# Optimization experiments

Measured on AMD Instinct MI355X. Metric: run time of the kernel, lower is better.

Reference implementation:

```python
import jax, jax.numpy as jnp
import numpy as np

B, D, E, H, K = 8192, 1024, 8, 4096, 2

def setup_inputs() -> dict:
    key = jax.random.key(0)
    ks = jax.random.split(key, 7)
    s_in = 1.0 / np.sqrt(D)
    s_hid = 1.0 / np.sqrt(H)
    return {
        "z":  jax.random.normal(ks[0], (B, D), dtype=jnp.float32),
        "Wg": jax.random.uniform(ks[1], (D, E), jnp.float32, -s_in, s_in),
        "bg": jnp.zeros((E,), jnp.float32),
        "W1": jax.random.uniform(ks[2], (E, D, H), jnp.float32, -s_in, s_in),
        "b1": jax.random.uniform(ks[3], (E, H), jnp.float32, -s_in, s_in),
        "W2": jax.random.uniform(ks[4], (E, H, D), jnp.float32, -s_hid, s_hid),
        "b2": jax.random.uniform(ks[5], (E, D), jnp.float32, -s_hid, s_hid),
    }

def reference(z, Wg, bg, W1, b1, W2, b2):
    # gate: softmax over experts, then keep only top-k weights (no renorm,
    # matching the original which sums topw * expert(z))
    w = jax.nn.softmax(z @ Wg + bg, axis=-1)            # [B, E]
    topw, idx = jax.lax.top_k(w, K)                      # [B, K] each
    wmask = jnp.zeros_like(w).at[jnp.arange(B)[:, None], idx].set(topw)  # [B, E]
    # dense all-expert MLP, then weighted combine (same math as per-token loop)
    h = jax.nn.relu(jnp.einsum('bd,edh->beh', z, W1) + b1)   # [B, E, H]
    y = jnp.einsum('beh,ehd->bed', h, W2) + b2               # [B, E, D]
    out = jnp.einsum('be,bed->bd', wmask, y)                 # [B, D]
    return out
```

## Files before the change

kernel.cpp:

```cpp
#include <hip/hip_runtime.h>
#include <hip/hip_bf16.h>
#include <cstdint>
#include <cstddef>

#define BTOK  8192
#define DIM   1024
#define NEXP  8
#define NHID  4096
#define HHALF 2048
#define GATE_TOK 64
#define ABASE (128 * 32)

typedef __bf16 bf16x8 __attribute__((ext_vector_type(8)));
typedef float  floatx4 __attribute__((ext_vector_type(4)));

#define O_COUNTS 0
#define O_BASE   256
#define O_TOKB   1024
#define O_TOKW   (O_TOKB + (size_t)NEXP*BTOK*4)
#define O_CE     (O_TOKW + (size_t)NEXP*BTOK*4)
#define O_CP     (O_CE + (size_t)2*BTOK*4)
#define O_CW     (O_CP + (size_t)2*BTOK*4)
#define O_ZBF    (O_CW + (size_t)2*BTOK*4)
#define O_W1T    (O_ZBF + (size_t)BTOK*DIM*2)
#define O_W2T    (O_W1T + (size_t)NEXP*DIM*NHID*2)
#define O_HBUF   (O_W2T + (size_t)NEXP*DIM*NHID*2)
#define WS_NEED  (O_HBUF + (size_t)2*BTOK*NHID*2)

__device__ __forceinline__ void gload_lds16(const void* g, void* l) {
  __builtin_amdgcn_global_load_lds(
      (const __attribute__((address_space(1))) void*)g,
      (__attribute__((address_space(3))) void*)l, 16, 0, 0);
}

__device__ __forceinline__ ushort f2bf(float x) {
  return __builtin_bit_cast(ushort, __float2bfloat16(x));
}

__global__ void k_zcnt(int* __restrict__ counts) {
  if (threadIdx.x < 12) counts[threadIdx.x] = 0;
}

__global__ void k_zout(float* __restrict__ out) {
  int i = blockIdx.x * blockDim.x + threadIdx.x;
  float4 z4 = {0.f, 0.f, 0.f, 0.f};
  float4* o = (float4*)out;
  int n = BTOK * DIM / 4;
  for (int j = i; j < n; j += gridDim.x * blockDim.x) o[j] = z4;
}

__global__ __launch_bounds__(256) void k_transpose(
    const float* __restrict__ src, __hip_bfloat16* __restrict__ dst, int R, int C) {
  __shared__ float tile[32][33];
  int zz = blockIdx.z;
  const float* s = src + (size_t)zz * R * C;
  __hip_bfloat16* d = dst + (size_t)zz * R * C;
  int c0 = blockIdx.x * 32, r0 = blockIdx.y * 32;
  int tx = threadIdx.x & 31, ty = threadIdx.x >> 5;
#pragma unroll
  for (int i = ty; i < 32; i += 8)
    tile[i][tx] = s[(size_t)(r0 + i) * C + c0 + tx];
  __syncthreads();
#pragma unroll
  for (int i = ty; i < 32; i += 8)
    d[(size_t)(c0 + i) * R + r0 + tx] = __float2bfloat16(tile[tx][i]);
}

__global__ __launch_bounds__(256) void k_gate(
    const float* __restrict__ z, const float* __restrict__ Wg,
    const float* __restrict__ bg, int* __restrict__ counts,
    int* __restrict__ tokb, float* __restrict__ tokw,
    __hip_bfloat16* __restrict__ zbf) {
  __shared__ float wgT[NEXP * DIM];
  __shared__ int   le[2 * GATE_TOK];
  __shared__ float lw[2 * GATE_TOK];
  __shared__ int   lr[2 * GATE_TOK];
  __shared__ int   lcnt[NEXP];
  __shared__ int   gbase[NEXP];

  int tid = threadIdx.x;
  if (tid < NEXP) lcnt[tid] = 0;
#pragma unroll
  for (int e = 0; e < NEXP; e++)
    for (int d = tid; d < DIM; d += 256)
      wgT[e * DIM + d] = Wg[d * NEXP + e];
  __syncthreads();

  int lane = tid & 63;
  int wv = tid >> 6;
  int b0 = blockIdx.x * GATE_TOK;

  for (int t = 0; t < 16; t++) {
    int lt = wv * 16 + t;
    int b = b0 + lt;
    const float4* zr4 = (const float4*)(z + (size_t)b * DIM);
    float4 zv[4];
#pragma unroll
    for (int i = 0; i < 4; i++) zv[i] = zr4[lane + 64 * i];
    ushort4* zb4 = (ushort4*)((ushort*)zbf + (size_t)b * DIM);
#pragma unroll
    for (int i = 0; i < 4; i++) {
      ushort4 u;
      u.x = f2bf(zv[i].x); u.y = f2bf(zv[i].y);
      u.z = f2bf(zv[i].z); u.w = f2bf(zv[i].w);
      zb4[lane + 64 * i] = u;
    }
    float acc[NEXP];
#pragma unroll
    for (int e = 0; e < NEXP; e++) acc[e] = 0.f;
#pragma unroll
    for (int e = 0; e < NEXP; e++) {
      const float4* wg4 = (const float4*)(wgT + e * DIM);
#pragma unroll
      for (int i = 0; i < 4; i++) {
        float4 w4 = wg4[lane + 64 * i];
        acc[e] += zv[i].x * w4.x + zv[i].y * w4.y + zv[i].z * w4.z + zv[i].w * w4.w;
      }
    }
#pragma unroll
    for (int off = 32; off > 0; off >>= 1) {
#pragma unroll
      for (int e = 0; e < NEXP; e++) acc[e] += __shfl_down(acc[e], off);
    }
    if (lane == 0) {
      float mx = -1e30f;
#pragma unroll
      for (int e = 0; e < NEXP; e++) { acc[e] += bg[e]; mx = fmaxf(mx, acc[e]); }
      float s = 0.f;
#pragma unroll
      for (int e = 0; e < NEXP; e++) { acc[e] = expf(acc[e] - mx); s += acc[e]; }
      float inv = 1.f / s;
      int i1 = -1, i2 = -1; float v1 = -1.f, v2 = -1.f;
#pragma unroll
      for (int e = 0; e < NEXP; e++) {
        float w = acc[e] * inv;
        if (w > v1) { v2 = v1; i2 = i1; v1 = w; i1 = e; }
        else if (w > v2) { v2 = w; i2 = e; }
      }
      le[2 * lt] = i1;     lw[2 * lt] = v1;
      le[2 * lt + 1] = i2; lw[2 * lt + 1] = v2;
    }
  }
  __syncthreads();
  if (tid < 2 * GATE_TOK) lr[tid] = atomicAdd(&lcnt[le[tid]], 1);
  __syncthreads();
  if (tid < NEXP) gbase[tid] = atomicAdd(&counts[tid], lcnt[tid]);
  __syncthreads();
  if (tid < 2 * GATE_TOK) {
    int e = le[tid];
    int p = gbase[e] + lr[tid];
    int b = b0 + (tid >> 1);
    tokb[e * BTOK + p] = b;
    tokw[e * BTOK + p] = lw[tid];
  }
}

__global__ void k_base(const int* __restrict__ counts, int* __restrict__ base) {
  if (threadIdx.x == 0 && blockIdx.x == 0) {
    int s = 0;
    for (int e = 0; e < NEXP; e++) { base[e] = s; s += counts[e]; }
    int a = 0, b = 0;
    base[8] = 0; base[17] = 0;
    for (int e = 0; e < NEXP; e++) {
      int mt = (counts[e] + 127) >> 7;
      a += mt * 16; b += mt * 4;
      base[9 + e] = a; base[18 + e] = b;
    }
  }
}


#define STG3(nxt_, tt_) do {                                                 \
    gload_lds16(srcA  + (tt_) * 32, &lds[nxt_][(wv * 16) * 32]);             \
    gload_lds16(srcB0 + (tt_) * 32, &lds[nxt_][ABASE + (wv * 16) * 32]);     \
    gload_lds16(srcB1 + (tt_) * 32, &lds[nxt_][ABASE + (128 + wv * 16) * 32]);\
  } while (0)

#define PH3(cur_, STG_, VM_) do {                                            \
    const ushort* Ab_ = &lds[cur_][0];                                       \
    const ushort* Bb_ = &lds[cur_][ABASE];                                   \
    bf16x8 afr_[4], bfr_[4];                                                 \
    _Pragma("unroll")                                                        \
    for (int j_ = 0; j_ < 4; j_++)                                           \
      bfr_[j_] = __builtin_bit_cast(bf16x8,                                  \
          *(const uint4*)(Bb_ + boff + j_ * 512));                           \
    _Pragma("unroll")                                                        \
    for (int i_ = 0; i_ < 4; i_++)                                           \
      afr_[i_] = __builtin_bit_cast(bf16x8,                                  \
          *(const uint4*)(Ab_ + aoff + i_ * 512));                           \
    STG_;                                                                    \
    __builtin_amdgcn_sched_barrier(0);                                       \
    VM_;                                                                     \
    __builtin_amdgcn_s_barrier();                                            \
    __builtin_amdgcn_sched_barrier(0);                                       \
    __builtin_amdgcn_s_setprio(1);                                           \
    _Pragma("unroll")                                                        \
    for (int i_ = 0; i_ < 4; i_++)                                           \
      _Pragma("unroll")                                                      \
      for (int j_ = 0; j_ < 4; j_++)                                         \
        acc[i_][j_] = __builtin_amdgcn_mfma_f32_16x16x32_bf16(               \
            afr_[i_], bfr_[j_], acc[i_][j_], 0, 0, 0);                       \
    __builtin_amdgcn_s_setprio(0);                                           \
    __builtin_amdgcn_sched_barrier(0);                                       \
    __builtin_amdgcn_s_barrier();                                            \
  } while (0)

#define VM3  asm volatile("s_waitcnt vmcnt(3)" ::: "memory")
#define VM0  asm volatile("s_waitcnt vmcnt(0)" ::: "memory")
#define NOP_ (void)0

__global__ __launch_bounds__(512, 4) void k_gemm1(
    const __hip_bfloat16* __restrict__ zbf, const __hip_bfloat16* __restrict__ w1t,
    const float* __restrict__ b1, const int* __restrict__ counts,
    const int* __restrict__ base, const int* __restrict__ tokb,
    __hip_bfloat16* __restrict__ hbuf,
    const int* __restrict__ tp, int* __restrict__ steal) {
  __shared__ __align__(16) ushort lds[3][(128 + 256) * 32];
  __shared__ int sh_g;

  int tid = threadIdx.x;
  int lane = tid & 63;
  int wv = tid >> 6;
  int wm = wv >> 2;
  int wn = wv & 3;
  int lrow = lane & 15;
  int quad = lane >> 4;
  int pc = quad ^ ((lrow >> 1) & 3);
  int aoff = (wm * 64 + lrow) * 32 + pc * 8;
  int boff = (wn * 64 + lrow) * 32 + pc * 8;
  int srow = wv * 16 + (lane >> 2);
  int sswz = ((lane & 3) ^ ((srow >> 1) & 3)) * 8;

  const ushort* zb = (const ushort*)zbf;
  const ushort* w1 = (const ushort*)w1t;
  const int NT = DIM / 32;
  int TT = tp[8];

  for (;;) {
    if (tid == 0) sh_g = atomicAdd(steal, 1);
    __syncthreads();
    int g = sh_g;
    if (g >= TT) break;

    int e = 0;
    while (g >= tp[e + 1]) e++;
    int local = g - tp[e];
    int mte = (tp[e + 1] - tp[e]) >> 4;
    int nt = local / mte;
    int mtl = local - nt * mte;
    int m0 = mtl * 128, n0 = nt * 256;
    int cnt = counts[e], gb = base[e];

    int m = m0 + srow; if (m >= cnt) m = cnt - 1;
    const ushort* srcA = zb + (size_t)tokb[e * BTOK + m] * DIM + sswz;
    const ushort* srcB0 = w1 + (size_t)(e * NHID + n0 + srow) * DIM + sswz;
    const ushort* srcB1 = w1 + (size_t)(e * NHID + n0 + 128 + srow) * DIM + sswz;

    STG3(0, 0);
    STG3(1, 1);
    VM3;
    __builtin_amdgcn_s_barrier();

    floatx4 acc[4][4];
#pragma unroll
    for (int i = 0; i < 4; i++)
#pragma unroll
      for (int j = 0; j < 4; j++) { floatx4 zf = {0.f,0.f,0.f,0.f}; acc[i][j] = zf; }

    int cur = 0;
#pragma unroll 1
    for (int t = 0; t < NT - 2; ++t) {
      int nxt = cur + 2; if (nxt >= 3) nxt -= 3;
      PH3(cur, STG3(nxt, t + 2), VM3);
      cur = (cur == 2) ? 0 : cur + 1;
    }
    PH3(cur, NOP_, VM0);
    cur = (cur == 2) ? 0 : cur + 1;
    PH3(cur, NOP_, NOP_);

    float bias[4];
#pragma unroll
    for (int j = 0; j < 4; j++)
      bias[j] = b1[e * NHID + n0 + wn * 64 + j * 16 + lrow];
    ushort* hp = (ushort*)hbuf;
#pragma unroll
    for (int i = 0; i < 4; i++) {
      int mloc = wm * 64 + i * 16 + quad * 4;
#pragma unroll
      for (int r = 0; r < 4; r++) {
        int mm = m0 + mloc + r;
        if (mm < cnt) {
          ushort* hr = hp + (size_t)(gb + mm) * NHID;
#pragma unroll
          for (int j = 0; j < 4; j++) {
            float v = fmaxf(acc[i][j][r] + bias[j], 0.f);
            hr[n0 + wn * 64 + j * 16 + lrow] = f2bf(v);
          }
        }
      }
    }
    __syncthreads();
  }
}

__global__ __launch_bounds__(512, 4) void k_gemm2(
    const __hip_bfloat16* __restrict__ hbuf, const __hip_bfloat16* __restrict__ w2t,
    const float* __restrict__ b2, const int* __restrict__ counts,
    const int* __restrict__ base, const int* __restrict__ tokb,
    const float* __restrict__ tokw, float* __restrict__ out,
    const int* __restrict__ tp, int* __restrict__ steal) {
  __shared__ __align__(16) ushort lds[3][(128 + 256) * 32];
  __shared__ int sh_g;

  int tid = threadIdx.x;
  int lane = tid & 63;
  int wv = tid >> 6;
  int wm = wv >> 2;
  int wn = wv & 3;
  int lrow = lane & 15;
  int quad = lane >> 4;
  int pc = quad ^ ((lrow >> 1) & 3);
  int aoff = (wm * 64 + lrow) * 32 + pc * 8;
  int boff = (wn * 64 + lrow) * 32 + pc * 8;
  int srow = wv * 16 + (lane >> 2);
  int sswz = ((lane & 3) ^ ((srow >> 1) & 3)) * 8;

  const ushort* hb = (const ushort*)hbuf;
  const ushort* w2 = (const ushort*)w2t;
  const int NT = HHALF / 32;
  int TT = tp[8];

  for (;;) {
    if (tid == 0) sh_g = atomicAdd(steal, 1);
    __syncthreads();
    int gu = sh_g;
    if (gu >= 2 * TT) break;
    int g = gu >> 1;
    int kseg = gu & 1;

    int e = 0;
    while (g >= tp[e + 1]) e++;
    int local = g - tp[e];
    int mte = (tp[e + 1] - tp[e]) >> 2;
    int nt = local / mte;
    int mtl = local - nt * mte;
    int m0 = mtl * 128, n0 = nt * 256;
    int cnt = counts[e], gb = base[e];

    int m = m0 + srow; if (m >= cnt) m = cnt - 1;
    const ushort* srcA = hb + (size_t)(gb + m) * NHID + kseg * HHALF + sswz;
    const ushort* srcB0 = w2 + (size_t)(e * DIM + n0 + srow) * NHID + kseg * HHALF + sswz;
    const ushort* srcB1 = w2 + (size_t)(e * DIM + n0 + 128 + srow) * NHID + kseg * HHALF + sswz;

    STG3(0, 0);
    STG3(1, 1);
    VM3;
    __builtin_amdgcn_s_barrier();

    floatx4 acc[4][4];
#pragma unroll
    for (int i = 0; i < 4; i++)
#pragma unroll
      for (int j = 0; j < 4; j++) { floatx4 zf = {0.f,0.f,0.f,0.f}; acc[i][j] = zf; }

    int cur = 0;
#pragma unroll 1
    for (int t = 0; t < NT - 2; ++t) {
      int nxt = cur + 2; if (nxt >= 3) nxt -= 3;
      PH3(cur, STG3(nxt, t + 2), VM3);
      cur = (cur == 2) ? 0 : cur + 1;
    }
    PH3(cur, NOP_, VM0);
    cur = (cur == 2) ? 0 : cur + 1;
    PH3(cur, NOP_, NOP_);

#pragma unroll
    for (int i = 0; i < 4; i++) {
      int mloc = wm * 64 + i * 16 + quad * 4;
#pragma unroll
      for (int r = 0; r < 4; r++) {
        int mm = m0 + mloc + r;
        if (mm < cnt) {
          int tk  = tokb[e * BTOK + mm];
          float w = tokw[e * BTOK + mm];
#pragma unroll
          for (int j = 0; j < 4; j++) {
            int n = n0 + wn * 64 + j * 16 + lrow;
            float v = acc[i][j][r] + (kseg == 0 ? b2[e * DIM + n] : 0.f);
            atomicAdd(&out[(size_t)tk * DIM + n], w * v);
          }
        }
      }
    }
    __syncthreads();
  }
}

extern "C" void kernel_launch(void* const* d_in, const int* in_sizes, int n_in,
                              void* d_out, int out_size, void* d_ws, size_t ws_size,
                              hipStream_t stream) {
  const float* z  = (const float*)d_in[0];
  const float* Wg = (const float*)d_in[1];
  const float* bg = (const float*)d_in[2];
  const float* W1 = (const float*)d_in[3];
  const float* b1 = (const float*)d_in[4];
  const float* W2 = (const float*)d_in[5];
  const float* b2 = (const float*)d_in[6];
  float* out = (float*)d_out;
  char* ws = (char*)d_ws;
  if (ws_size < WS_NEED) return;

  int*   counts = (int*)(ws + O_COUNTS);
  int*   base   = (int*)(ws + O_BASE);
  int*   tokb   = (int*)(ws + O_TOKB);
  float* tokw   = (float*)(ws + O_TOKW);
  __hip_bfloat16* zbf  = (__hip_bfloat16*)(ws + O_ZBF);
  __hip_bfloat16* w1t  = (__hip_bfloat16*)(ws + O_W1T);
  __hip_bfloat16* w2t  = (__hip_bfloat16*)(ws + O_W2T);
  __hip_bfloat16* hbuf = (__hip_bfloat16*)(ws + O_HBUF);

  k_zcnt<<<1, 64, 0, stream>>>(counts);
  k_zout<<<512, 256, 0, stream>>>(out);
  k_transpose<<<dim3(NHID / 32, DIM / 32, NEXP), 256, 0, stream>>>(W1, w1t, DIM, NHID);
  k_transpose<<<dim3(DIM / 32, NHID / 32, NEXP), 256, 0, stream>>>(W2, w2t, NHID, DIM);
  k_gate<<<BTOK / GATE_TOK, 256, 0, stream>>>(z, Wg, bg, counts, tokb, tokw, zbf);
  k_base<<<1, 64, 0, stream>>>(counts, base);
  k_gemm1<<<512, 512, 0, stream>>>(
      zbf, w1t, b1, counts, base, tokb, hbuf, base + 8, counts + 8);
  k_gemm2<<<512, 512, 0, stream>>>(
      hbuf, w2t, b2, counts, base, tokb, tokw, out, base + 17, counts + 9);
}
```

Measured before the change: 879.3 us.

## Shrink GEMM tiles to 128x128 with 4-wave blocks and restructure LDS pipeline

Both expert GEMMs change from 512-thread blocks computing 128x256 tiles to 256-thread blocks computing 128x128 tiles. There are twice as many tiles, the persistent grid grows to 768 blocks, and the per-expert tile prefix counts in k_base are updated to match. Each stage now issues four 16-byte global-to-LDS loads per thread, and the wait and barrier move ahead of the fragment reads with adjusted vmcnt thresholds. The aim is finer load balance and more independent blocks per CU. The cost is lower reuse of each loaded A/B tile, so more global traffic per FLOP.

```diff
diff --git a/kernel.cpp b/kernel.cpp
--- a/kernel.cpp
+++ b/kernel.cpp
@@ -163,20 +163,26 @@
     base[8] = 0; base[17] = 0;
     for (int e = 0; e < NEXP; e++) {
       int mt = (counts[e] + 127) >> 7;
-      a += mt * 16; b += mt * 4;
+      a += mt * 32; b += mt * 8;
       base[9 + e] = a; base[18 + e] = b;
     }
   }
 }
 
 
-#define STG3(nxt_, tt_) do {                                                 \
-    gload_lds16(srcA  + (tt_) * 32, &lds[nxt_][(wv * 16) * 32]);             \
-    gload_lds16(srcB0 + (tt_) * 32, &lds[nxt_][ABASE + (wv * 16) * 32]);     \
-    gload_lds16(srcB1 + (tt_) * 32, &lds[nxt_][ABASE + (128 + wv * 16) * 32]);\
+#define STG4(nxt_, tt_) do {                                                  \
+    gload_lds16(srcA0 + (tt_) * 32, &lds[nxt_][(wv * 16) * 32]);              \
+    gload_lds16(srcA1 + (tt_) * 32, &lds[nxt_][(64 + wv * 16) * 32]);         \
+    gload_lds16(srcB0 + (tt_) * 32, &lds[nxt_][ABASE + (wv * 16) * 32]);      \
+    gload_lds16(srcB1 + (tt_) * 32, &lds[nxt_][ABASE + (64 + wv * 16) * 32]); \
   } while (0)
 
-#define PH3(cur_, STG_, VM_) do {                                            \
+#define PHR(cur_, STG_, VM_) do {                                            \
+    STG_;                                                                    \
+    __builtin_amdgcn_sched_barrier(0);                                       \
+    VM_;                                                                     \
+    __builtin_amdgcn_s_barrier();                                            \
+    __builtin_amdgcn_sched_barrier(0);                                       \
     const ushort* Ab_ = &lds[cur_][0];                                       \
     const ushort* Bb_ = &lds[cur_][ABASE];                                   \
     bf16x8 afr_[4], bfr_[4];                                                 \
@@ -188,11 +194,6 @@
     for (int i_ = 0; i_ < 4; i_++)                                           \
       afr_[i_] = __builtin_bit_cast(bf16x8,                                  \
           *(const uint4*)(Ab_ + aoff + i_ * 512));                           \
-    STG_;                                                                    \
-    __builtin_amdgcn_sched_barrier(0);                                       \
-    VM_;                                                                     \
-    __builtin_amdgcn_s_barrier();                                            \
-    __builtin_amdgcn_sched_barrier(0);                                       \
     __builtin_amdgcn_s_setprio(1);                                           \
     _Pragma("unroll")                                                        \
     for (int i_ = 0; i_ < 4; i_++)                                           \
@@ -205,24 +206,25 @@
     __builtin_amdgcn_s_barrier();                                            \
   } while (0)
 
-#define VM3  asm volatile("s_waitcnt vmcnt(3)" ::: "memory")
+#define VM8  asm volatile("s_waitcnt vmcnt(8)" ::: "memory")
+#define VM4  asm volatile("s_waitcnt vmcnt(4)" ::: "memory")
 #define VM0  asm volatile("s_waitcnt vmcnt(0)" ::: "memory")
 #define NOP_ (void)0
 
-__global__ __launch_bounds__(512, 4) void k_gemm1(
+__global__ __launch_bounds__(256, 3) void k_gemm1(
     const __hip_bfloat16* __restrict__ zbf, const __hip_bfloat16* __restrict__ w1t,
     const float* __restrict__ b1, const int* __restrict__ counts,
     const int* __restrict__ base, const int* __restrict__ tokb,
     __hip_bfloat16* __restrict__ hbuf,
     const int* __restrict__ tp, int* __restrict__ steal) {
-  __shared__ __align__(16) ushort lds[3][(128 + 256) * 32];
+  __shared__ __align__(16) ushort lds[3][(128 + 128) * 32];
   __shared__ int sh_g;
 
   int tid = threadIdx.x;
   int lane = tid & 63;
   int wv = tid >> 6;
-  int wm = wv >> 2;
-  int wn = wv & 3;
+  int wm = wv >> 1;
+  int wn = wv & 1;
   int lrow = lane & 15;
   int quad = lane >> 4;
   int pc = quad ^ ((lrow >> 1) & 3);
@@ -245,21 +247,21 @@
     int e = 0;
     while (g >= tp[e + 1]) e++;
     int local = g - tp[e];
-    int mte = (tp[e + 1] - tp[e]) >> 4;
+    int mte = (tp[e + 1] - tp[e]) >> 5;
     int nt = local / mte;
     int mtl = local - nt * mte;
-    int m0 = mtl * 128, n0 = nt * 256;
+    int m0 = mtl * 128, n0 = nt * 128;
     int cnt = counts[e], gb = base[e];
 
-    int m = m0 + srow; if (m >= cnt) m = cnt - 1;
-    const ushort* srcA = zb + (size_t)tokb[e * BTOK + m] * DIM + sswz;
+    int ma = m0 + srow;      if (ma >= cnt) ma = cnt - 1;
+    int mb = m0 + 64 + srow; if (mb >= cnt) mb = cnt - 1;
+    const ushort* srcA0 = zb + (size_t)tokb[e * BTOK + ma] * DIM + sswz;
+    const ushort* srcA1 = zb + (size_t)tokb[e * BTOK + mb] * DIM + sswz;
     const ushort* srcB0 = w1 + (size_t)(e * NHID + n0 + srow) * DIM + sswz;
-    const ushort* srcB1 = w1 + (size_t)(e * NHID + n0 + 128 + srow) * DIM + sswz;
-
-    STG3(0, 0);
-    STG3(1, 1);
-    VM3;
-    __builtin_amdgcn_s_barrier();
+    const ushort* srcB1 = w1 + (size_t)(e * NHID + n0 + 64 + srow) * DIM + sswz;
+
+    STG4(0, 0);
+    STG4(1, 1);
 
     floatx4 acc[4][4];
 #pragma unroll
@@ -271,12 +273,12 @@
 #pragma unroll 1
     for (int t = 0; t < NT - 2; ++t) {
       int nxt = cur + 2; if (nxt >= 3) nxt -= 3;
-      PH3(cur, STG3(nxt, t + 2), VM3);
+      PHR(cur, STG4(nxt, t + 2), VM8);
       cur = (cur == 2) ? 0 : cur + 1;
     }
-    PH3(cur, NOP_, VM0);
+    PHR(cur, NOP_, VM4);
     cur = (cur == 2) ? 0 : cur + 1;
-    PH3(cur, NOP_, NOP_);
+    PHR(cur, NOP_, VM0);
 
     float bias[4];
 #pragma unroll
@@ -303,20 +305,20 @@
   }
 }
 
-__global__ __launch_bounds__(512, 4) void k_gemm2(
+__global__ __launch_bounds__(256, 3) void k_gemm2(
     const __hip_bfloat16* __restrict__ hbuf, const __hip_bfloat16* __restrict__ w2t,
     const float* __restrict__ b2, const int* __restrict__ counts,
     const int* __restrict__ base, const int* __restrict__ tokb,
     const float* __restrict__ tokw, float* __restrict__ out,
     const int* __restrict__ tp, int* __restrict__ steal) {
-  __shared__ __align__(16) ushort lds[3][(128 + 256) * 32];
+  __shared__ __align__(16) ushort lds[3][(128 + 128) * 32];
   __shared__ int sh_g;
 
   int tid = threadIdx.x;
   int lane = tid & 63;
   int wv = tid >> 6;
-  int wm = wv >> 2;
-  int wn = wv & 3;
+  int wm = wv >> 1;
+  int wn = wv & 1;
   int lrow = lane & 15;
   int quad = lane >> 4;
   int pc = quad ^ ((lrow >> 1) & 3);
@@ -341,21 +343,21 @@
     int e = 0;
     while (g >= tp[e + 1]) e++;
     int local = g - tp[e];
-    int mte = (tp[e + 1] - tp[e]) >> 2;
+    int mte = (tp[e + 1] - tp[e]) >> 3;
     int nt = local / mte;
     int mtl = local - nt * mte;
-    int m0 = mtl * 128, n0 = nt * 256;
+    int m0 = mtl * 128, n0 = nt * 128;
     int cnt = counts[e], gb = base[e];
 
-    int m = m0 + srow; if (m >= cnt) m = cnt - 1;
-    const ushort* srcA = hb + (size_t)(gb + m) * NHID + kseg * HHALF + sswz;
+    int ma = m0 + srow;      if (ma >= cnt) ma = cnt - 1;
+    int mb = m0 + 64 + srow; if (mb >= cnt) mb = cnt - 1;
+    const ushort* srcA0 = hb + (size_t)(gb + ma) * NHID + kseg * HHALF + sswz;
+    const ushort* srcA1 = hb + (size_t)(gb + mb) * NHID + kseg * HHALF + sswz;
     const ushort* srcB0 = w2 + (size_t)(e * DIM + n0 + srow) * NHID + kseg * HHALF + sswz;
-    const ushort* srcB1 = w2 + (size_t)(e * DIM + n0 + 128 + srow) * NHID + kseg * HHALF + sswz;
-
-    STG3(0, 0);
-    STG3(1, 1);
-    VM3;
-    __builtin_amdgcn_s_barrier();
+    const ushort* srcB1 = w2 + (size_t)(e * DIM + n0 + 64 + srow) * NHID + kseg * HHALF + sswz;
+
+    STG4(0, 0);
+    STG4(1, 1);
 
     floatx4 acc[4][4];
 #pragma unroll
@@ -367,12 +369,12 @@
 #pragma unroll 1
     for (int t = 0; t < NT - 2; ++t) {
       int nxt = cur + 2; if (nxt >= 3) nxt -= 3;
-      PH3(cur, STG3(nxt, t + 2), VM3);
+      PHR(cur, STG4(nxt, t + 2), VM8);
       cur = (cur == 2) ? 0 : cur + 1;
     }
-    PH3(cur, NOP_, VM0);
+    PHR(cur, NOP_, VM4);
     cur = (cur == 2) ? 0 : cur + 1;
-    PH3(cur, NOP_, NOP_);
+    PHR(cur, NOP_, VM0);
 
 #pragma unroll
     for (int i = 0; i < 4; i++) {
@@ -425,8 +427,8 @@
   k_transpose<<<dim3(DIM / 32, NHID / 32, NEXP), 256, 0, stream>>>(W2, w2t, NHID, DIM);
   k_gate<<<BTOK / GATE_TOK, 256, 0, stream>>>(z, Wg, bg, counts, tokb, tokw, zbf);
   k_base<<<1, 64, 0, stream>>>(counts, base);
-  k_gemm1<<<512, 512, 0, stream>>>(
+  k_gemm1<<<768, 256, 0, stream>>>(
       zbf, w1t, b1, counts, base, tokb, hbuf, base + 8, counts + 8);
-  k_gemm2<<<512, 512, 0, stream>>>(
+  k_gemm2<<<768, 256, 0, stream>>>(
       hbuf, w2t, b2, counts, base, tokb, tokw, out, base + 17, counts + 9);
 }
```

Result: slower. 912.1 us (+3.7%).
